# Optimization experiments

Measured on AMD Instinct MI355X. Metric: run time of the kernel, lower is better.

Reference implementation:

```python
import jax, jax.numpy as jnp
import numpy as np

N, E = 20000, 320000
IN_C, HID, OUT_C, HEADS = 512, 32, 40, 8
NEG_SLOPE = 0.2


def setup_inputs() -> dict:
    key = jax.random.key(0)
    ks = jax.random.split(key, 10)
    x = jax.random.normal(ks[0], (N, IN_C), dtype=jnp.float32)
    edge_index = jax.random.randint(ks[1], (2, E), 0, N, dtype=jnp.int64)
    s1 = 1.0 / np.sqrt(IN_C)
    s2 = 1.0 / np.sqrt(HEADS * HID)
    return {
        "x": x,
        "edge_index": edge_index,
        "w1": jax.random.normal(ks[2], (IN_C, HEADS * HID), dtype=jnp.float32) * s1,
        "att_src1": jax.random.normal(ks[3], (HEADS, HID), dtype=jnp.float32) * s2,
        "att_dst1": jax.random.normal(ks[4], (HEADS, HID), dtype=jnp.float32) * s2,
        "b1": jnp.zeros((HEADS * HID,), dtype=jnp.float32),
        "w2": jax.random.normal(ks[5], (HEADS * HID, OUT_C), dtype=jnp.float32) * s2,
        "att_src2": jax.random.normal(ks[6], (1, OUT_C), dtype=jnp.float32) * 0.15,
        "att_dst2": jax.random.normal(ks[7], (1, OUT_C), dtype=jnp.float32) * 0.15,
        "b2": jnp.zeros((OUT_C,), dtype=jnp.float32),
    }


def gat_conv(x, src, dst, w, att_src, att_dst, bias, heads, out_c, concat):
    n = x.shape[0]
    h = (x @ w).reshape(n, heads, out_c)            # [N,H,C]
    a_s = jnp.sum(h * att_src, axis=-1)             # [N,H]
    a_d = jnp.sum(h * att_dst, axis=-1)             # [N,H]
    e = jax.nn.leaky_relu(a_s[src] + a_d[dst], NEG_SLOPE)  # [E,H]
    # segment softmax over destination nodes (self-loops guarantee nonempty)
    m = jax.ops.segment_max(e, dst, num_segments=n)
    e = jnp.exp(e - m[dst])
    z = jax.ops.segment_sum(e, dst, num_segments=n)
    alpha = e / (z[dst] + 1e-16)                    # [E,H]
    msg = alpha[:, :, None] * h[src]                # [E,H,C]
    out = jax.ops.segment_sum(msg, dst, num_segments=n)  # [N,H,C]
    out = out.reshape(n, heads * out_c) if concat else out.mean(axis=1)
    return out + bias


def reference(x, edge_index, w1, att_src1, att_dst1, b1, w2, att_src2, att_dst2, b2):
    n = x.shape[0]
    loops = jnp.arange(n, dtype=edge_index.dtype)
    src = jnp.concatenate([edge_index[0], loops])
    dst = jnp.concatenate([edge_index[1], loops])
    h = gat_conv(x, src, dst, w1, att_src1, att_dst1, b1, HEADS, HID, True)
    h = jax.nn.elu(h)
    out = gat_conv(h, src, dst, w2, att_src2, att_dst2, b2, 1, OUT_C, False)
    return jax.nn.log_softmax(out, axis=1)
```

## Files before the change

kernel.cpp:

```cpp
#include <hip/hip_runtime.h>
#include <hip/hip_bf16.h>
#include <math.h>

#define N_NODES 20000
#define N_EDGES 320000
#define ET (N_EDGES + N_NODES)
#define IN_C 512
#define HEADS 8
#define HID 32
#define HH (HEADS * HID)
#define OUT_C 40
#define NEG_SLOPE 0.2f

typedef __attribute__((ext_vector_type(8))) short short8;
typedef __attribute__((ext_vector_type(4))) float floatx4;

static __device__ __forceinline__ unsigned short f2bf(float f) {
  __hip_bfloat16 h = __float2bfloat16(f);
  return *(unsigned short*)&h;
}
static __device__ __forceinline__ float bf2f_lo(unsigned int u) {
  return __uint_as_float(u << 16);
}
static __device__ __forceinline__ float bf2f_hi(unsigned int u) {
  return __uint_as_float(u & 0xFFFF0000u);
}

#define WCONV_BLOCKS (IN_C * HH / 256)
#define W2CONV_BLOCKS (HH * OUT_C / 256)
#define COUNT_BLOCKS ((ET + 255) / 256)
__global__ __launch_bounds__(256) void prep_kernel(
    const float* __restrict__ w1, const float* __restrict__ w2,
    const int* __restrict__ ei, unsigned short* __restrict__ wbT,
    unsigned short* __restrict__ w2bT, int* __restrict__ deg) {
  if (blockIdx.x < WCONV_BLOCKS) {
    int j = blockIdx.x * 256 + threadIdx.x;
    int k = j >> 8, n = j & 255;
    wbT[(size_t)n * IN_C + k] = f2bf(w1[j]);
  } else if (blockIdx.x < WCONV_BLOCKS + W2CONV_BLOCKS) {
    int j = (blockIdx.x - WCONV_BLOCKS) * 256 + threadIdx.x;
    int k = j / OUT_C, oc = j % OUT_C;
    w2bT[oc * HH + k] = f2bf(w2[j]);
  } else {
    int e = (blockIdx.x - WCONV_BLOCKS - W2CONV_BLOCKS) * 256 + threadIdx.x;
    if (e < ET) {
      int dst = (e < N_EDGES) ? ei[N_EDGES + e] : (e - N_EDGES);
      atomicAdd(&deg[dst], 1);
    }
  }
}

#define BM 64
#define BN 128
#define BK 32
#define APAD 40
#define GY ((N_NODES + BM - 1) / BM)
#define GEMM_BLOCKS (2 * GY)
__global__ __launch_bounds__(256) void gemm1_kernel(
    const float* __restrict__ X, const unsigned short* __restrict__ BT,
    const float* __restrict__ bias, unsigned short* __restrict__ C,
    const int* __restrict__ deg, int* __restrict__ offs, int* __restrict__ cursor) {
  if (blockIdx.x >= GEMM_BLOCKS) {
    __shared__ int wsum[4];
    int t = threadIdx.x;
    int4 buf[20];
    int s = 0;
    if (t < 250) {
      const int4* dp = (const int4*)deg + t * 20;
#pragma unroll
      for (int i = 0; i < 20; i++) {
        buf[i] = dp[i];
        s += buf[i].x + buf[i].y + buf[i].z + buf[i].w;
      }
    }
    int lane = t & 63, w = t >> 6;
    int inc = s;
    for (int o = 1; o < 64; o <<= 1) {
      int u = __shfl_up(inc, o, 64);
      if (lane >= o) inc += u;
    }
    if (lane == 63) wsum[w] = inc;
    __syncthreads();
    int waveOff = 0;
    for (int i = 0; i < w; i++) waveOff += wsum[i];
    int running = waveOff + inc - s;
    if (t < 250) {
      int base = t * 80;
#pragma unroll
      for (int i = 0; i < 20; i++) {
        int4 v = buf[i];
        int4 o;
        o.x = running;
        o.y = o.x + v.x;
        o.z = o.y + v.y;
        o.w = o.z + v.z;
        running = o.w + v.w;
        *(int4*)(offs + base + i * 4) = o;
        *(int4*)(cursor + base + i * 4) = o;
      }
    }
    if (t == 0) offs[N_NODES] = ET;
    return;
  }
  __shared__ unsigned short As[BM][APAD];
  __shared__ unsigned short Bs[BN][APAD];
  const int tid = threadIdx.x;
  const int lane = tid & 63, wave = tid >> 6;
  const int wm = (wave & 1) * 32;
  const int wn = (wave >> 1) * 64;
  const int r16 = lane & 15, q = lane >> 4;
  const int bx = blockIdx.x & 1, by = blockIdx.x >> 1;
  const int rowBase = by * BM;
  const int colBase = bx * BN;
  floatx4 acc[2][4] = {};

  for (int k0 = 0; k0 < IN_C; k0 += BK) {
    {
      int row = tid >> 2, kc = (tid & 3) * 8;
      int arow = rowBase + row;
      float4 v0 = make_float4(0.f, 0.f, 0.f, 0.f), v1 = v0;
      if (arow < N_NODES) {
        const float* p = X + (size_t)arow * IN_C + k0 + kc;
        v0 = *(const float4*)p;
        v1 = *(const float4*)(p + 4);
      }
      unsigned short tmp[8] = {f2bf(v0.x), f2bf(v0.y), f2bf(v0.z), f2bf(v0.w),
                               f2bf(v1.x), f2bf(v1.y), f2bf(v1.z), f2bf(v1.w)};
      *(float4*)&As[row][kc] = *(const float4*)tmp;
    }
#pragma unroll
    for (int i = 0; i < 2; i++) {
      int c = tid + i * 256;
      int row = c >> 2, kc = (c & 3) * 8;
      float4 v = *(const float4*)(BT + (size_t)(colBase + row) * IN_C + k0 + kc);
      *(float4*)&Bs[row][kc] = v;
    }
    __syncthreads();
    short8 afrag[2], bfrag[4];
#pragma unroll
    for (int mt = 0; mt < 2; mt++)
      afrag[mt] = *(const short8*)&As[wm + mt * 16 + r16][q * 8];
#pragma unroll
    for (int nt = 0; nt < 4; nt++)
      bfrag[nt] = *(const short8*)&Bs[wn + nt * 16 + r16][q * 8];
#pragma unroll
    for (int mt = 0; mt < 2; mt++)
#pragma unroll
      for (int nt = 0; nt < 4; nt++)
        acc[mt][nt] = __builtin_amdgcn_mfma_f32_16x16x32_bf16(
            afrag[mt], bfrag[nt], acc[mt][nt], 0, 0, 0);
    __syncthreads();
  }
#pragma unroll
  for (int mt = 0; mt < 2; mt++) {
#pragma unroll
    for (int nt = 0; nt < 4; nt++) {
      int col = colBase + wn + nt * 16 + r16;
      float bb = bias[col];
#pragma unroll
      for (int r = 0; r < 4; r++) {
        int row = rowBase + wm + mt * 16 + q * 4 + r;
        if (row < N_NODES) C[(size_t)row * HH + col] = f2bf(acc[mt][nt][r] + bb);
      }
    }
  }
}

#define FILL_BLOCKS ((ET + 255) / 256)
#define ATTN1_BLOCKS (N_NODES / 4)
__global__ __launch_bounds__(256) void fill_attn1_kernel(
    const int* __restrict__ ei, int* __restrict__ cursor, int* __restrict__ csr,
    const unsigned short* __restrict__ h1b, const float* __restrict__ asrc,
    const float* __restrict__ adst, float* __restrict__ as1, float* __restrict__ ad1) {
  if (blockIdx.x < FILL_BLOCKS) {
    int e = blockIdx.x * 256 + threadIdx.x;
    if (e >= ET) return;
    int src, dst;
    if (e < N_EDGES) { src = ei[e]; dst = ei[N_EDGES + e]; }
    else { src = e - N_EDGES; dst = src; }
    int pos = atomicAdd(&cursor[dst], 1);
    csr[pos] = src;
  } else {
    int wave = threadIdx.x >> 6, lane = threadIdx.x & 63;
    int n = (blockIdx.x - FILL_BLOCKS) * 4 + wave;
    int c4 = lane * 4;
    uint2 raw = *(const uint2*)(h1b + (size_t)n * HH + c4);
    float h0 = bf2f_lo(raw.x), h1 = bf2f_hi(raw.x);
    float h2 = bf2f_lo(raw.y), h3 = bf2f_hi(raw.y);
    float4 sa = *(const float4*)(asrc + c4);
    float4 sd = *(const float4*)(adst + c4);
    float ps = h0 * sa.x + h1 * sa.y + h2 * sa.z + h3 * sa.w;
    float pd = h0 * sd.x + h1 * sd.y + h2 * sd.z + h3 * sd.w;
#pragma unroll
    for (int o = 4; o > 0; o >>= 1) {
      ps += __shfl_down(ps, o, 8);
      pd += __shfl_down(pd, o, 8);
    }
    if ((lane & 7) == 0) {
      as1[n * HEADS + (lane >> 3)] = ps;
      ad1[n * HEADS + (lane >> 3)] = pd;
    }
  }
}

#define NPB 16
#define H2ROW 264
__global__ __launch_bounds__(256) void layer1_fused_kernel(
    const unsigned short* __restrict__ h1b, const float* __restrict__ as1,
    const float* __restrict__ ad1, const int* __restrict__ offs,
    const int* __restrict__ csr, const float* __restrict__ b1,
    const unsigned short* __restrict__ w2bT, const float* __restrict__ b2,
    const float* __restrict__ asrc2, const float* __restrict__ adst2,
    float* __restrict__ h3, float* __restrict__ as2, float* __restrict__ ad2) {
  __shared__ __align__(16) unsigned short h2s[NPB][H2ROW];
  __shared__ float psum[3][NPB], pdsum[3][NPB];
  const int tid = threadIdx.x;
  const int wave = tid >> 6, lane = tid & 63;
  const int r16 = lane & 15, q = lane >> 4;
  const int nodeBase = blockIdx.x * NPB;

  const int strm = lane >> 5;
  const int l32 = lane & 31;
  const int c8 = l32 * 8;
  const int head = l32 >> 2;
  float4 bb = *(const float4*)(b1 + c8 + strm * 4);
  for (int i = 0; i < 4; i++) {
    int local = wave * 4 + i;
    int n = nodeBase + local;
    int beg = offs[n], end = offs[n + 1];
    float ad = ad1[n * HEADS + head];
    float acc[8] = {};
    float l = 0.f;
    int k = beg + strm;
    if (k < end) {
      int src = csr[k];
      uint4 r = *(const uint4*)(h1b + ((unsigned)src << 8) + c8);
      float e = as1[src * HEADS + head];
      for (k += 2; k < end; k += 2) {
        int src2 = csr[k];
        uint4 r2 = *(const uint4*)(h1b + ((unsigned)src2 << 8) + c8);
        float e2 = as1[src2 * HEADS + head];
        float t = e + ad;
        t = (t > 0.f) ? t : NEG_SLOPE * t;
        float p = __expf(t);
        l += p;
        acc[0] = fmaf(p, bf2f_lo(r.x), acc[0]);
        acc[1] = fmaf(p, bf2f_hi(r.x), acc[1]);
        acc[2] = fmaf(p, bf2f_lo(r.y), acc[2]);
        acc[3] = fmaf(p, bf2f_hi(r.y), acc[3]);
        acc[4] = fmaf(p, bf2f_lo(r.z), acc[4]);
        acc[5] = fmaf(p, bf2f_hi(r.z), acc[5]);
        acc[6] = fmaf(p, bf2f_lo(r.w), acc[6]);
        acc[7] = fmaf(p, bf2f_hi(r.w), acc[7]);
        r = r2; e = e2;
      }
      float t = e + ad;
      t = (t > 0.f) ? t : NEG_SLOPE * t;
      float p = __expf(t);
      l += p;
      acc[0] = fmaf(p, bf2f_lo(r.x), acc[0]);
      acc[1] = fmaf(p, bf2f_hi(r.x), acc[1]);
      acc[2] = fmaf(p, bf2f_lo(r.y), acc[2]);
      acc[3] = fmaf(p, bf2f_hi(r.y), acc[3]);
      acc[4] = fmaf(p, bf2f_lo(r.z), acc[4]);
      acc[5] = fmaf(p, bf2f_hi(r.z), acc[5]);
      acc[6] = fmaf(p, bf2f_lo(r.w), acc[6]);
      acc[7] = fmaf(p, bf2f_hi(r.w), acc[7]);
    }
#pragma unroll
    for (int j = 0; j < 8; j++) acc[j] += __shfl_xor(acc[j], 32, 64);
    l += __shfl_xor(l, 32, 64);
    float li = 1.f / (l + 1e-16f);
    float v0 = (strm ? acc[4] : acc[0]) * li + bb.x;
    float v1 = (strm ? acc[5] : acc[1]) * li + bb.y;
    float v2 = (strm ? acc[6] : acc[2]) * li + bb.z;
    float v3 = (strm ? acc[7] : acc[3]) * li + bb.w;
    v0 = (v0 > 0.f) ? v0 : __expf(v0) - 1.f;
    v1 = (v1 > 0.f) ? v1 : __expf(v1) - 1.f;
    v2 = (v2 > 0.f) ? v2 : __expf(v2) - 1.f;
    v3 = (v3 > 0.f) ? v3 : __expf(v3) - 1.f;
    uint2 w;
    w.x = (unsigned)f2bf(v0) | ((unsigned)f2bf(v1) << 16);
    w.y = (unsigned)f2bf(v2) | ((unsigned)f2bf(v3) << 16);
    *(uint2*)&h2s[local][c8 + strm * 4] = w;
  }
  __syncthreads();

  if (wave < 3) {
    int col = wave * 16 + r16;
    int colc = (col < OUT_C) ? col : 0;
    short8 bfrag[8];
#pragma unroll
    for (int s = 0; s < 8; s++)
      bfrag[s] = *(const short8*)(w2bT + colc * HH + s * 32 + q * 8);
    float sa = 0.f, sd = 0.f, b2c = 0.f;
    if (col < OUT_C) { sa = asrc2[col]; sd = adst2[col]; b2c = b2[col]; }
    floatx4 dacc = {};
#pragma unroll
    for (int s = 0; s < 8; s++) {
      short8 afrag = *(const short8*)&h2s[r16][s * 32 + q * 8];
      dacc = __builtin_amdgcn_mfma_f32_16x16x32_bf16(afrag, bfrag[s], dacc, 0, 0, 0);
    }
    float psr[4], pdr[4];
#pragma unroll
    for (int r = 0; r < 4; r++) {
      float val = dacc[r] + b2c;
      if (col < OUT_C)
        h3[(size_t)(nodeBase + q * 4 + r) * OUT_C + col] = val;
      psr[r] = val * sa;
      pdr[r] = val * sd;
    }
#pragma unroll
    for (int o = 8; o > 0; o >>= 1) {
#pragma unroll
      for (int r = 0; r < 4; r++) {
        psr[r] += __shfl_down(psr[r], o, 16);
        pdr[r] += __shfl_down(pdr[r], o, 16);
      }
    }
    if (r16 == 0) {
#pragma unroll
      for (int r = 0; r < 4; r++) {
        psum[wave][q * 4 + r] = psr[r];
        pdsum[wave][q * 4 + r] = pdr[r];
      }
    }
  }
  __syncthreads();
  if (tid < NPB) {
    as2[nodeBase + tid] = psum[0][tid] + psum[1][tid] + psum[2][tid];
    ad2[nodeBase + tid] = pdsum[0][tid] + pdsum[1][tid] + pdsum[2][tid];
  }
}

__global__ __launch_bounds__(256) void agg2_kernel(
    const float* __restrict__ h3, const float* __restrict__ as2,
    const float* __restrict__ ad2, const int* __restrict__ offs,
    const int* __restrict__ csr, const float* __restrict__ b2,
    float* __restrict__ out) {
  int n = blockIdx.x * 4 + (threadIdx.x >> 6);
  int t = threadIdx.x & 63;
  bool act = (t < OUT_C);
  int beg = offs[n], end = offs[n + 1];
  float ad = ad2[n];
  float l0 = 0.f, l1 = 0.f, a0 = 0.f, a1 = 0.f;
  int k = beg;
  for (; k + 1 < end; k += 2) {
    int s0 = csr[k], s1 = csr[k + 1];
    float e0 = as2[s0] + ad, e1 = as2[s1] + ad;
    e0 = (e0 > 0.f) ? e0 : NEG_SLOPE * e0;
    e1 = (e1 > 0.f) ? e1 : NEG_SLOPE * e1;
    float p0 = __expf(e0), p1 = __expf(e1);
    l0 += p0; l1 += p1;
    float h0 = act ? h3[(size_t)s0 * OUT_C + t] : 0.f;
    float h1 = act ? h3[(size_t)s1 * OUT_C + t] : 0.f;
    a0 = fmaf(p0, h0, a0);
    a1 = fmaf(p1, h1, a1);
  }
  if (k < end) {
    int s0 = csr[k];
    float e0 = as2[s0] + ad;
    e0 = (e0 > 0.f) ? e0 : NEG_SLOPE * e0;
    float p0 = __expf(e0);
    l0 += p0;
    float h0 = act ? h3[(size_t)s0 * OUT_C + t] : 0.f;
    a0 = fmaf(p0, h0, a0);
  }
  float l = l0 + l1, acc = a0 + a1;
  float v = acc / (l + 1e-16f) + (act ? b2[t] : 0.f);
  float x = act ? v : -INFINITY;
  float mx = x;
  for (int o = 32; o > 0; o >>= 1) mx = fmaxf(mx, __shfl_down(mx, o, 64));
  mx = __shfl(mx, 0, 64);
  float ex = act ? __expf(v - mx) : 0.f;
  float s = ex;
  for (int o = 32; o > 0; o >>= 1) s += __shfl_down(s, o, 64);
  s = __shfl(s, 0, 64);
  if (act) out[(size_t)n * OUT_C + t] = v - mx - logf(s);
}

extern "C" void kernel_launch(void* const* d_in, const int* in_sizes, int n_in,
                              void* d_out, int out_size, void* d_ws, size_t ws_size,
                              hipStream_t stream) {
  const float* x     = (const float*)d_in[0];
  const int*   ei    = (const int*)d_in[1];
  const float* w1    = (const float*)d_in[2];
  const float* asrc1 = (const float*)d_in[3];
  const float* adst1 = (const float*)d_in[4];
  const float* b1    = (const float*)d_in[5];
  const float* w2    = (const float*)d_in[6];
  const float* asrc2 = (const float*)d_in[7];
  const float* adst2 = (const float*)d_in[8];
  const float* b2    = (const float*)d_in[9];
  float* out = (float*)d_out;

  float* fw = (float*)d_ws;
  float* as1   = fw;  fw += (size_t)N_NODES * HEADS;
  float* ad1   = fw;  fw += (size_t)N_NODES * HEADS;
  float* h3    = fw;  fw += (size_t)N_NODES * OUT_C;
  float* as2   = fw;  fw += N_NODES;
  float* ad2   = fw;  fw += N_NODES;
  unsigned short* h1b  = (unsigned short*)fw;  fw += (size_t)N_NODES * HH / 2;
  unsigned short* wbT  = (unsigned short*)fw;  fw += (size_t)IN_C * HH / 2;
  unsigned short* w2bT = (unsigned short*)fw;  fw += (size_t)HH * OUT_C / 2;
  int* deg    = (int*)fw;
  int* offs   = deg + N_NODES;
  int* cursor = offs + N_NODES + 4;
  int* csr    = cursor + N_NODES;

  hipMemsetAsync(deg, 0, N_NODES * sizeof(int), stream);

  prep_kernel<<<WCONV_BLOCKS + W2CONV_BLOCKS + COUNT_BLOCKS, 256, 0, stream>>>(
      w1, w2, ei, wbT, w2bT, deg);
  gemm1_kernel<<<GEMM_BLOCKS + 1, 256, 0, stream>>>(x, wbT, b1, h1b, deg, offs, cursor);
  fill_attn1_kernel<<<FILL_BLOCKS + ATTN1_BLOCKS, 256, 0, stream>>>(
      ei, cursor, csr, h1b, asrc1, adst1, as1, ad1);
  layer1_fused_kernel<<<N_NODES / NPB, 256, 0, stream>>>(
      h1b, as1, ad1, offs, csr, b1, w2bT, b2, asrc2, adst2, h3, as2, ad2);
  agg2_kernel<<<N_NODES / 4, 256, 0, stream>>>(h3, as2, ad2, offs, csr, b2, out);
}
```

Before: 220.3 us.

## Double waves per block in layer-1 aggregation, batch CSR index loads, unroll agg2

The fused layer-1 kernel now launches 512 threads (8 waves) per block, so each wave aggregates 2 nodes instead of 4. Within each node, neighbor indices are loaded 64 at a time with one coalesced read and passed to lanes by shuffle, instead of each lane issuing its own scalar CSR read. The layer-2 aggregation loop is unrolled by 4 with independent accumulators, so more gather loads are in flight at once. The aim is more memory-level parallelism on the irregular gathers. The risks are higher register pressure under the new launch bounds, and that the unchanged second half of the fused kernel (the per-wave projection and partial-sum step) may assume only 4 waves.

```diff
diff --git a/kernel.cpp b/kernel.cpp
--- a/kernel.cpp
+++ b/kernel.cpp
@@ -205,7 +205,7 @@
 
 #define NPB 16
 #define H2ROW 264
-__global__ __launch_bounds__(256) void layer1_fused_kernel(
+__global__ __launch_bounds__(512, 8) void layer1_fused_kernel(
     const unsigned short* __restrict__ h1b, const float* __restrict__ as1,
     const float* __restrict__ ad1, const int* __restrict__ offs,
     const int* __restrict__ csr, const float* __restrict__ b1,
@@ -224,25 +224,44 @@
   const int c8 = l32 * 8;
   const int head = l32 >> 2;
   float4 bb = *(const float4*)(b1 + c8 + strm * 4);
-  for (int i = 0; i < 4; i++) {
-    int local = wave * 4 + i;
+#pragma unroll
+  for (int i = 0; i < 2; i++) {
+    int local = wave * 2 + i;
     int n = nodeBase + local;
     int beg = offs[n], end = offs[n + 1];
+    int cnt = end - beg;
     float ad = ad1[n * HEADS + head];
     float acc[8] = {};
     float l = 0.f;
-    int k = beg + strm;
-    if (k < end) {
-      int src = csr[k];
-      uint4 r = *(const uint4*)(h1b + ((unsigned)src << 8) + c8);
-      float e = as1[src * HEADS + head];
-      for (k += 2; k < end; k += 2) {
-        int src2 = csr[k];
-        uint4 r2 = *(const uint4*)(h1b + ((unsigned)src2 << 8) + c8);
-        float e2 = as1[src2 * HEADS + head];
-        float t = e + ad;
-        t = (t > 0.f) ? t : NEG_SLOPE * t;
-        float p = __expf(t);
+    for (int kb = 0; kb < cnt; kb += 64) {
+      int nb = (cnt - kb < 64) ? (cnt - kb) : 64;
+      int myidx = (lane < nb) ? csr[beg + kb + lane] : 0;
+      int j = strm;
+      if (j < nb) {
+        int src = __shfl(myidx, j, 64);
+        uint4 r = *(const uint4*)(h1b + ((unsigned)src << 8) + c8);
+        float e = as1[src * HEADS + head];
+        for (j += 2; j < nb; j += 2) {
+          int src2 = __shfl(myidx, j, 64);
+          uint4 r2 = *(const uint4*)(h1b + ((unsigned)src2 << 8) + c8);
+          float e2 = as1[src2 * HEADS + head];
+          float tt = e + ad;
+          tt = (tt > 0.f) ? tt : NEG_SLOPE * tt;
+          float p = __expf(tt);
+          l += p;
+          acc[0] = fmaf(p, bf2f_lo(r.x), acc[0]);
+          acc[1] = fmaf(p, bf2f_hi(r.x), acc[1]);
+          acc[2] = fmaf(p, bf2f_lo(r.y), acc[2]);
+          acc[3] = fmaf(p, bf2f_hi(r.y), acc[3]);
+          acc[4] = fmaf(p, bf2f_lo(r.z), acc[4]);
+          acc[5] = fmaf(p, bf2f_hi(r.z), acc[5]);
+          acc[6] = fmaf(p, bf2f_lo(r.w), acc[6]);
+          acc[7] = fmaf(p, bf2f_hi(r.w), acc[7]);
+          r = r2; e = e2;
+        }
+        float tt = e + ad;
+        tt = (tt > 0.f) ? tt : NEG_SLOPE * tt;
+        float p = __expf(tt);
         l += p;
         acc[0] = fmaf(p, bf2f_lo(r.x), acc[0]);
         acc[1] = fmaf(p, bf2f_hi(r.x), acc[1]);
@@ -252,20 +271,7 @@
         acc[5] = fmaf(p, bf2f_hi(r.z), acc[5]);
         acc[6] = fmaf(p, bf2f_lo(r.w), acc[6]);
         acc[7] = fmaf(p, bf2f_hi(r.w), acc[7]);
-        r = r2; e = e2;
-      }
-      float t = e + ad;
-      t = (t > 0.f) ? t : NEG_SLOPE * t;
-      float p = __expf(t);
-      l += p;
-      acc[0] = fmaf(p, bf2f_lo(r.x), acc[0]);
-      acc[1] = fmaf(p, bf2f_hi(r.x), acc[1]);
-      acc[2] = fmaf(p, bf2f_lo(r.y), acc[2]);
-      acc[3] = fmaf(p, bf2f_hi(r.y), acc[3]);
-      acc[4] = fmaf(p, bf2f_lo(r.z), acc[4]);
-      acc[5] = fmaf(p, bf2f_hi(r.z), acc[5]);
-      acc[6] = fmaf(p, bf2f_lo(r.w), acc[6]);
-      acc[7] = fmaf(p, bf2f_hi(r.w), acc[7]);
+      }
     }
 #pragma unroll
     for (int j = 0; j < 8; j++) acc[j] += __shfl_xor(acc[j], 32, 64);
@@ -343,21 +349,29 @@
   bool act = (t < OUT_C);
   int beg = offs[n], end = offs[n + 1];
   float ad = ad2[n];
-  float l0 = 0.f, l1 = 0.f, a0 = 0.f, a1 = 0.f;
+  float l0 = 0.f, l1 = 0.f, l2 = 0.f, l3 = 0.f;
+  float a0 = 0.f, a1 = 0.f, a2 = 0.f, a3 = 0.f;
   int k = beg;
-  for (; k + 1 < end; k += 2) {
-    int s0 = csr[k], s1 = csr[k + 1];
+  for (; k + 3 < end; k += 4) {
+    int s0 = csr[k], s1 = csr[k + 1], s2 = csr[k + 2], s3 = csr[k + 3];
     float e0 = as2[s0] + ad, e1 = as2[s1] + ad;
+    float e2 = as2[s2] + ad, e3 = as2[s3] + ad;
     e0 = (e0 > 0.f) ? e0 : NEG_SLOPE * e0;
     e1 = (e1 > 0.f) ? e1 : NEG_SLOPE * e1;
-    float p0 = __expf(e0), p1 = __expf(e1);
-    l0 += p0; l1 += p1;
+    e2 = (e2 > 0.f) ? e2 : NEG_SLOPE * e2;
+    e3 = (e3 > 0.f) ? e3 : NEG_SLOPE * e3;
+    float p0 = __expf(e0), p1 = __expf(e1), p2 = __expf(e2), p3 = __expf(e3);
+    l0 += p0; l1 += p1; l2 += p2; l3 += p3;
     float h0 = act ? h3[(size_t)s0 * OUT_C + t] : 0.f;
     float h1 = act ? h3[(size_t)s1 * OUT_C + t] : 0.f;
+    float h2 = act ? h3[(size_t)s2 * OUT_C + t] : 0.f;
+    float h3v = act ? h3[(size_t)s3 * OUT_C + t] : 0.f;
     a0 = fmaf(p0, h0, a0);
     a1 = fmaf(p1, h1, a1);
-  }
-  if (k < end) {
+    a2 = fmaf(p2, h2, a2);
+    a3 = fmaf(p3, h3v, a3);
+  }
+  for (; k < end; k++) {
     int s0 = csr[k];
     float e0 = as2[s0] + ad;
     e0 = (e0 > 0.f) ? e0 : NEG_SLOPE * e0;
@@ -366,7 +380,7 @@
     float h0 = act ? h3[(size_t)s0 * OUT_C + t] : 0.f;
     a0 = fmaf(p0, h0, a0);
   }
-  float l = l0 + l1, acc = a0 + a1;
+  float l = (l0 + l1) + (l2 + l3), acc = (a0 + a1) + (a2 + a3);
   float v = acc / (l + 1e-16f) + (act ? b2[t] : 0.f);
   float x = act ? v : -INFINITY;
   float mx = x;
@@ -415,7 +429,7 @@
   gemm1_kernel<<<GEMM_BLOCKS + 1, 256, 0, stream>>>(x, wbT, b1, h1b, deg, offs, cursor);
   fill_attn1_kernel<<<FILL_BLOCKS + ATTN1_BLOCKS, 256, 0, stream>>>(
       ei, cursor, csr, h1b, asrc1, adst1, as1, ad1);
-  layer1_fused_kernel<<<N_NODES / NPB, 256, 0, stream>>>(
+  layer1_fused_kernel<<<N_NODES / NPB, 512, 0, stream>>>(
       h1b, as1, ad1, offs, csr, b1, w2bT, b2, asrc2, adst2, h3, as2, ad2);
   agg2_kernel<<<N_NODES / 4, 256, 0, stream>>>(h3, as2, ad2, offs, csr, b2, out);
 }
```

New measurement: 208.9 us. 5.2% less time.
